# Kernel tuning notes

Measured on AMD Instinct MI355X. Metric: run time of the kernel, lower is better.

## Reference

```python
import jax, jax.numpy as jnp
import numpy as np

N, E = 50000, 800000
IN, HID, OUT, K = 500, 128, 128, 10
BN_EPS = 1e-5


def _encode(x, src, dst, norm, n, W_in, b_in, gam, high_pass, bn_scale, bn_shift, W_up, b_up):
    # input projection (dropout_p = 0 -> identity)
    h = x @ W_in + b_in  # [N, HID]

    def prop(t):
        # symmetric-normalized sparse matvec: (D^-1/2 A D^-1/2) t
        return jax.ops.segment_sum(norm[:, None] * t[src], dst, num_segments=n)

    def step(carry, g):
        t, acc = carry
        acc = acc + g * t
        pt = prop(t)
        # low-pass basis: A_hat^k x ; high-pass basis: (I - A_hat)^k x
        t = (t - pt) if high_pass else pt
        return (t, acc), None

    (_, acc), _ = jax.lax.scan(step, (h, jnp.zeros_like(h)), gam)

    # BatchNorm1d over the node axis (training-mode batch statistics)
    mu = acc.mean(axis=0)
    var = acc.var(axis=0)
    hn = (acc - mu) * jax.lax.rsqrt(var + BN_EPS) * bn_scale + bn_shift
    z = hn @ W_up + b_up
    return jax.nn.relu(z)  # act_fn='relu' (PolyGCL default)


def setup_inputs() -> dict:
    key = jax.random.key(0)
    ks = jax.random.split(key, 4)
    x = jax.random.normal(ks[0], (N, IN), dtype=jnp.float32)
    edge_index = jax.random.randint(ks[1], (2, E), 0, N, dtype=jnp.int32)
    W_in = jax.random.normal(ks[2], (IN, HID), dtype=jnp.float32) * (1.0 / np.sqrt(IN))
    b_in = jnp.zeros((HID,), dtype=jnp.float32)
    # low-pass: decreasing coefficients; high-pass: increasing (PolyGCL init scheme)
    gamma_L = jnp.linspace(2.0, 0.0, K + 1, dtype=jnp.float32)
    gamma_H = jnp.linspace(0.0, 2.0, K + 1, dtype=jnp.float32)
    bn_scale = jnp.ones((HID,), dtype=jnp.float32)
    bn_shift = jnp.zeros((HID,), dtype=jnp.float32)
    W_up = jax.random.normal(ks[3], (HID, OUT), dtype=jnp.float32) * (1.0 / np.sqrt(HID))
    b_up = jnp.zeros((OUT,), dtype=jnp.float32)
    return {"x": x, "edge_index": edge_index, "W_in": W_in, "b_in": b_in,
            "gamma_L": gamma_L, "gamma_H": gamma_H,
            "bn_scale": bn_scale, "bn_shift": bn_shift,
            "W_up": W_up, "b_up": b_up}


def reference(x, edge_index, W_in, b_in, gamma_L, gamma_H, bn_scale, bn_shift, W_up, b_up):
    n = x.shape[0]
    src, dst = edge_index[0], edge_index[1]
    deg = jax.ops.segment_sum(jnp.ones(src.shape, dtype=x.dtype), dst, num_segments=n)
    dinv = jax.lax.rsqrt(jnp.maximum(deg, 1.0))
    norm = dinv[src] * dinv[dst]  # [E]
    Z_L = _encode(x, src, dst, norm, n, W_in, b_in, gamma_L, False, bn_scale, bn_shift, W_up, b_up)
    Z_H = _encode(x, src, dst, norm, n, W_in, b_in, gamma_H, True, bn_scale, bn_shift, W_up, b_up)
    return (Z_L, Z_H)
```

## Files before the change

kernel.cpp:

```cpp
#include <hip/hip_runtime.h>
#include <hip/hip_fp16.h>

#define HIDF 128

typedef float v4f __attribute__((ext_vector_type(4)));
typedef _Float16 half8 __attribute__((ext_vector_type(8)));
typedef float f32x4 __attribute__((ext_vector_type(4)));
struct alignas(8) half4 { __half2 lo, hi; };

static inline int cdiv(int a, int b) { return (a + b - 1) / b; }
static inline size_t alup(size_t b) { return (b + 255) & ~(size_t)255; }

__global__ void k_deg(const int* __restrict__ dst, int E, int* __restrict__ deg) {
    int i = blockIdx.x * blockDim.x + threadIdx.x;
    if (i < E) atomicAdd(&deg[dst[i]], 1);
}

__global__ void k_coef(const float* __restrict__ gL, const float* __restrict__ gH, int K,
                       float* __restrict__ cL, float* __restrict__ cH) {
    if (threadIdx.x == 0 && blockIdx.x == 0) {
        for (int j = 0; j <= K; ++j) {
            double s = 0.0;
            double C = 1.0;
            for (int k = j; k <= K; ++k) {
                s += (double)gH[k] * C;
                C = C * (double)(k + 1) / (double)(k + 1 - j);
            }
            cH[j] = (j & 1) ? (float)(-s) : (float)s;
            cL[j] = gL[j];
        }
    }
}

__global__ __launch_bounds__(256) void k_scan1(const int* __restrict__ deg, int N,
                                               int* __restrict__ bsum,
                                               float* __restrict__ dinv) {
    __shared__ int ls[256];
    int tid = threadIdx.x;
    int i = blockIdx.x * 256 + tid;
    int v = 0;
    if (i < N) {
        v = deg[i];
        dinv[i] = rsqrtf(fmaxf((float)v, 1.0f));
    }
    ls[tid] = v;
    __syncthreads();
    for (int off = 128; off > 0; off >>= 1) {
        if (tid < off) ls[tid] += ls[tid + off];
        __syncthreads();
    }
    if (tid == 0) bsum[blockIdx.x] = ls[0];
}

__global__ __launch_bounds__(1024) void k_scan2(int* __restrict__ bsum, int nb) {
    __shared__ int ls[1024];
    int tid = threadIdx.x;
    int v = (tid < nb) ? bsum[tid] : 0;
    ls[tid] = v;
    __syncthreads();
    for (int off = 1; off < 1024; off <<= 1) {
        int t = (tid >= off) ? ls[tid - off] : 0;
        __syncthreads();
        ls[tid] += t;
        __syncthreads();
    }
    if (tid < nb) bsum[tid] = ls[tid] - v;
}

__global__ __launch_bounds__(256) void k_scan3(const int* __restrict__ deg,
                                               const int* __restrict__ bsum, int N,
                                               int* __restrict__ row_ptr) {
    __shared__ int ls[256];
    int tid = threadIdx.x;
    int i = blockIdx.x * 256 + tid;
    int v = (i < N) ? deg[i] : 0;
    ls[tid] = v;
    __syncthreads();
    for (int off = 1; off < 256; off <<= 1) {
        int t = (tid >= off) ? ls[tid - off] : 0;
        __syncthreads();
        ls[tid] += t;
        __syncthreads();
    }
    if (i <= N) row_ptr[i] = bsum[blockIdx.x] + ls[tid] - v;
}

__global__ __launch_bounds__(1024) void k_scan(const int* __restrict__ deg, int N,
                                               int* __restrict__ row_ptr,
                                               float* __restrict__ dinv) {
    __shared__ int ls[1024];
    int tid = threadIdx.x;
    int chunk = (N + 1023) / 1024;
    int start = tid * chunk;
    int end = min(start + chunk, N);
    int s = 0;
    for (int i = start; i < end; ++i) {
        int d = deg[i];
        s += d;
        dinv[i] = rsqrtf(fmaxf((float)d, 1.0f));
    }
    ls[tid] = s;
    __syncthreads();
    for (int off = 1; off < 1024; off <<= 1) {
        int v = (tid >= off) ? ls[tid - off] : 0;
        __syncthreads();
        ls[tid] += v;
        __syncthreads();
    }
    int run = ls[tid] - s;
    for (int i = start; i < end; ++i) {
        row_ptr[i] = run;
        run += deg[i];
    }
    if (tid == 1023) row_ptr[N] = run;
}

__global__ void k_scatter(const int* __restrict__ src, const int* __restrict__ dst, int E,
                          const int* __restrict__ row_ptr, int* __restrict__ fill,
                          const float* __restrict__ dinv, int* __restrict__ csr_src,
                          float* __restrict__ csr_w) {
    int i = blockIdx.x * blockDim.x + threadIdx.x;
    if (i < E) {
        int s = src[i], d = dst[i];
        int pos = row_ptr[d] + atomicAdd(&fill[d], 1);
        csr_src[pos] = s;
        csr_w[pos] = dinv[s] * dinv[d];
    }
}

__global__ __launch_bounds__(512) void k_wprep(const float* __restrict__ W, int Kdim, int KP,
                                               _Float16* __restrict__ Wh,
                                               _Float16* __restrict__ Wl) {
    int i = blockIdx.x * blockDim.x + threadIdx.x;
    int total = 128 * KP;
    if (i >= total) return;
    int n = i / KP;
    int k = i - n * KP;
    float w = (k < Kdim) ? W[(long)k * HIDF + n] : 0.0f;
    _Float16 h = (_Float16)w;
    _Float16 l = (_Float16)(w - (float)h);
    Wh[(long)n * KP + k] = h;
    Wl[(long)n * KP + k] = l;
}

__global__ __launch_bounds__(512) void k_gemm_in_mfma(
    const float* __restrict__ X, const _Float16* __restrict__ Wh,
    const _Float16* __restrict__ Wl, const float* __restrict__ b, __half* __restrict__ U0,
    int M, int Kdim, int KP) {
    __shared__ _Float16 Ah[128][40];
    __shared__ _Float16 Al[128][40];
    __shared__ _Float16 Bh[128][40];
    __shared__ _Float16 Bl[128][40];
    int tid = threadIdx.x;
    int lane = tid & 63;
    int wid = tid >> 6;
    int wr = wid >> 1;
    int wc = wid & 1;
    int lr = lane & 15;
    int kq = lane >> 4;
    int kof = kq * 8;
    int row0 = blockIdx.x * 128;
    int sm = tid >> 2;
    int kk = (tid & 3) * 8;
    bool k4ok = ((Kdim & 3) == 0);

    f32x4 acc[2][4] = {};

    for (int k0 = 0; k0 < KP; k0 += 32) {
        *(half8*)&Bh[sm][kk] = *(const half8*)&Wh[(long)sm * KP + k0 + kk];
        *(half8*)&Bl[sm][kk] = *(const half8*)&Wl[(long)sm * KP + k0 + kk];
        {
            int r = row0 + sm;
            int gk = k0 + kk;
            half8 hv, lv;
            if (r < M && (gk + 8) <= Kdim && k4ok) {
                float4 v0 = *(const float4*)&X[(long)r * Kdim + gk];
                float4 v1 = *(const float4*)&X[(long)r * Kdim + gk + 4];
                float xs[8] = {v0.x, v0.y, v0.z, v0.w, v1.x, v1.y, v1.z, v1.w};
#pragma unroll
                for (int j = 0; j < 8; ++j) {
                    _Float16 h = (_Float16)xs[j];
                    hv[j] = h;
                    lv[j] = (_Float16)(xs[j] - (float)h);
                }
            } else {
#pragma unroll
                for (int j = 0; j < 8; ++j) {
                    float x = (r < M && (gk + j) < Kdim) ? X[(long)r * Kdim + gk + j] : 0.0f;
                    _Float16 h = (_Float16)x;
                    hv[j] = h;
                    lv[j] = (_Float16)(x - (float)h);
                }
            }
            *(half8*)&Ah[sm][kk] = hv;
            *(half8*)&Al[sm][kk] = lv;
        }
        __syncthreads();

        half8 a_h0 = *(const half8*)&Ah[wr * 32 + lr][kof];
        half8 a_h1 = *(const half8*)&Ah[wr * 32 + 16 + lr][kof];
        half8 a_l0 = *(const half8*)&Al[wr * 32 + lr][kof];
        half8 a_l1 = *(const half8*)&Al[wr * 32 + 16 + lr][kof];
#pragma unroll
        for (int cg = 0; cg < 4; ++cg) {
            half8 b_h = *(const half8*)&Bh[wc * 64 + cg * 16 + lr][kof];
            half8 b_l = *(const half8*)&Bl[wc * 64 + cg * 16 + lr][kof];
            acc[0][cg] = __builtin_amdgcn_mfma_f32_16x16x32_f16(a_h0, b_h, acc[0][cg], 0, 0, 0);
            acc[1][cg] = __builtin_amdgcn_mfma_f32_16x16x32_f16(a_h1, b_h, acc[1][cg], 0, 0, 0);
            acc[0][cg] = __builtin_amdgcn_mfma_f32_16x16x32_f16(a_l0, b_h, acc[0][cg], 0, 0, 0);
            acc[1][cg] = __builtin_amdgcn_mfma_f32_16x16x32_f16(a_l1, b_h, acc[1][cg], 0, 0, 0);
            acc[0][cg] = __builtin_amdgcn_mfma_f32_16x16x32_f16(a_h0, b_l, acc[0][cg], 0, 0, 0);
            acc[1][cg] = __builtin_amdgcn_mfma_f32_16x16x32_f16(a_h1, b_l, acc[1][cg], 0, 0, 0);
        }
        __syncthreads();
    }

    float bb[4];
#pragma unroll
    for (int cg = 0; cg < 4; ++cg) bb[cg] = b[wc * 64 + cg * 16 + lr];
#pragma unroll
    for (int i = 0; i < 2; ++i) {
#pragma unroll
        for (int j = 0; j < 4; ++j) {
            int r = row0 + wr * 32 + i * 16 + kq * 4 + j;
            if (r < M) {
#pragma unroll
                for (int cg = 0; cg < 4; ++cg) {
                    int n = wc * 64 + cg * 16 + lr;
                    U0[(long)r * HIDF + n] = __float2half(acc[i][cg][j] + bb[cg]);
                }
            }
        }
    }
}

__global__ __launch_bounds__(512) void k_gemm_up_mfma(
    const float* __restrict__ accL, const float* __restrict__ accH,
    const _Float16* __restrict__ Wh, const _Float16* __restrict__ Wl,
    const float* __restrict__ bias, const float* __restrict__ a_mul,
    const float* __restrict__ aaW, float* __restrict__ out, int M) {
    int enc = blockIdx.y;
    const float* A = enc ? accH : accL;
    float* O = out + (size_t)enc * M * HIDF;
    __shared__ _Float16 Ah[128][40];
    __shared__ _Float16 Al[128][40];
    __shared__ _Float16 Bh[128][40];
    __shared__ _Float16 Bl[128][40];
    __shared__ float ams[128];
    int tid = threadIdx.x;
    int lane = tid & 63;
    int wid = tid >> 6;
    int wr = wid >> 1;
    int wc = wid & 1;
    int lr = lane & 15;
    int kq = lane >> 4;
    int kof = kq * 8;
    int row0 = blockIdx.x * 128;
    int sm = tid >> 2;
    int kk = (tid & 3) * 8;
    if (tid < 128) ams[tid] = a_mul[enc * 128 + tid];
    __syncthreads();

    f32x4 acc[2][4] = {};

    for (int k0 = 0; k0 < 128; k0 += 32) {
        *(half8*)&Bh[sm][kk] = *(const half8*)&Wh[(long)sm * 128 + k0 + kk];
        *(half8*)&Bl[sm][kk] = *(const half8*)&Wl[(long)sm * 128 + k0 + kk];
        {
            int r = row0 + sm;
            half8 hv, lv;
            if (r < M) {
                float4 v0 = *(const float4*)&A[(long)r * 128 + k0 + kk];
                float4 v1 = *(const float4*)&A[(long)r * 128 + k0 + kk + 4];
                float xs[8] = {v0.x, v0.y, v0.z, v0.w, v1.x, v1.y, v1.z, v1.w};
#pragma unroll
                for (int j = 0; j < 8; ++j) {
                    float sv = xs[j] * ams[k0 + kk + j];
                    _Float16 h = (_Float16)sv;
                    hv[j] = h;
                    lv[j] = (_Float16)(sv - (float)h);
                }
            } else {
#pragma unroll
                for (int j = 0; j < 8; ++j) { hv[j] = (_Float16)0.f; lv[j] = (_Float16)0.f; }
            }
            *(half8*)&Ah[sm][kk] = hv;
            *(half8*)&Al[sm][kk] = lv;
        }
        __syncthreads();

        half8 a_h0 = *(const half8*)&Ah[wr * 32 + lr][kof];
        half8 a_h1 = *(const half8*)&Ah[wr * 32 + 16 + lr][kof];
        half8 a_l0 = *(const half8*)&Al[wr * 32 + lr][kof];
        half8 a_l1 = *(const half8*)&Al[wr * 32 + 16 + lr][kof];
#pragma unroll
        for (int cg = 0; cg < 4; ++cg) {
            half8 b_h = *(const half8*)&Bh[wc * 64 + cg * 16 + lr][kof];
            half8 b_l = *(const half8*)&Bl[wc * 64 + cg * 16 + lr][kof];
            acc[0][cg] = __builtin_amdgcn_mfma_f32_16x16x32_f16(a_h0, b_h, acc[0][cg], 0, 0, 0);
            acc[1][cg] = __builtin_amdgcn_mfma_f32_16x16x32_f16(a_h1, b_h, acc[1][cg], 0, 0, 0);
            acc[0][cg] = __builtin_amdgcn_mfma_f32_16x16x32_f16(a_l0, b_h, acc[0][cg], 0, 0, 0);
            acc[1][cg] = __builtin_amdgcn_mfma_f32_16x16x32_f16(a_l1, b_h, acc[1][cg], 0, 0, 0);
            acc[0][cg] = __builtin_amdgcn_mfma_f32_16x16x32_f16(a_h0, b_l, acc[0][cg], 0, 0, 0);
            acc[1][cg] = __builtin_amdgcn_mfma_f32_16x16x32_f16(a_h1, b_l, acc[1][cg], 0, 0, 0);
        }
        __syncthreads();
    }

    float bb[4];
#pragma unroll
    for (int cg = 0; cg < 4; ++cg) {
        int n = wc * 64 + cg * 16 + lr;
        bb[cg] = bias[n] + aaW[enc * 128 + n];
    }
#pragma unroll
    for (int i = 0; i < 2; ++i) {
#pragma unroll
        for (int j = 0; j < 4; ++j) {
            int r = row0 + wr * 32 + i * 16 + kq * 4 + j;
            if (r < M) {
#pragma unroll
                for (int cg = 0; cg < 4; ++cg) {
                    int n = wc * 64 + cg * 16 + lr;
                    O[(long)r * HIDF + n] = fmaxf(acc[i][cg][j] + bb[cg], 0.0f);
                }
            }
        }
    }
}

__global__ __launch_bounds__(512) void k_gemm_in_f(
    const float* __restrict__ X, const float* __restrict__ W, const float* __restrict__ b,
    float* __restrict__ H, float* __restrict__ accL, float* __restrict__ accH,
    const float* __restrict__ cL, const float* __restrict__ cH, int M, int Kdim) {
    const int BK = 20;
    __shared__ float As[BK][132];
    __shared__ float Bs[BK][128];
    int tid = threadIdx.x;
    int tx = tid & 31, ty = tid >> 5;
    int row0 = blockIdx.x * 128;
    float acc[8][4] = {};
    for (int k0 = 0; k0 < Kdim; k0 += BK) {
        for (int l = tid; l < 640; l += 512) {
            int m = l / 5, q = l % 5;
            int r = row0 + m;
            float4 v = {0.f, 0.f, 0.f, 0.f};
            if (r < M) v = *(const float4*)&X[(long)r * Kdim + k0 + q * 4];
            As[q * 4 + 0][m] = v.x;
            As[q * 4 + 1][m] = v.y;
            As[q * 4 + 2][m] = v.z;
            As[q * 4 + 3][m] = v.w;
        }
        for (int l = tid; l < 640; l += 512) {
            int k = l >> 5, n = (l & 31) * 4;
            *(float4*)&Bs[k][n] = *(const float4*)&W[(long)(k0 + k) * 128 + n];
        }
        __syncthreads();
#pragma unroll
        for (int k = 0; k < BK; ++k) {
            float4 a0 = *(const float4*)&As[k][ty * 8];
            float4 a1 = *(const float4*)&As[k][ty * 8 + 4];
            float4 bb = *(const float4*)&Bs[k][tx * 4];
            float a[8] = {a0.x, a0.y, a0.z, a0.w, a1.x, a1.y, a1.z, a1.w};
#pragma unroll
            for (int i = 0; i < 8; ++i) {
                acc[i][0] += a[i] * bb.x;
                acc[i][1] += a[i] * bb.y;
                acc[i][2] += a[i] * bb.z;
                acc[i][3] += a[i] * bb.w;
            }
        }
        __syncthreads();
    }
    float g0 = cL[0], h0 = cH[0];
    float4 bias = *(const float4*)&b[tx * 4];
    float bv[4] = {bias.x, bias.y, bias.z, bias.w};
#pragma unroll
    for (int i = 0; i < 8; ++i) {
        int r = row0 + ty * 8 + i;
        if (r < M) {
            long idx = (long)r * 128 + tx * 4;
            float4 vh;
            float* ph = (float*)&vh;
#pragma unroll
            for (int j = 0; j < 4; ++j) ph[j] = acc[i][j] + bv[j];
            *(float4*)&H[idx] = vh;
            float4 vl = {g0 * vh.x, g0 * vh.y, g0 * vh.z, g0 * vh.w};
            float4 vv = {h0 * vh.x, h0 * vh.y, h0 * vh.z, h0 * vh.w};
            *(float4*)&accL[idx] = vl;
            *(float4*)&accH[idx] = vv;
        }
    }
}

__global__ __launch_bounds__(256) void k_prop_h(
    const int* __restrict__ row_ptr, const int* __restrict__ csr_src,
    const float* __restrict__ csr_w, const __half* __restrict__ t_in,
    __half* __restrict__ t_out, int N) {
    int wave = threadIdx.x >> 6;
    int lane = threadIdx.x & 63;
    int half = lane >> 5;
    int l5 = lane & 31;
    int node = blockIdx.x * 4 + wave;
    if (node >= N) return;
    int e0 = row_ptr[node], e1 = row_ptr[node + 1];
    float sx = 0.f, sy = 0.f, sz = 0.f, sw = 0.f;
    int e = e0 + half;
    for (; e + 14 < e1; e += 16) {
        int idx[8];
        float w[8];
        half4 v[8];
#pragma unroll
        for (int q = 0; q < 8; ++q) {
            idx[q] = csr_src[e + 2 * q];
            w[q] = csr_w[e + 2 * q];
        }
#pragma unroll
        for (int q = 0; q < 8; ++q) v[q] = *(const half4*)&t_in[(long)idx[q] * HIDF + l5 * 4];
#pragma unroll
        for (int q = 0; q < 8; ++q) {
            float2 a = __half22float2(v[q].lo), b2 = __half22float2(v[q].hi);
            sx += w[q] * a.x;
            sy += w[q] * a.y;
            sz += w[q] * b2.x;
            sw += w[q] * b2.y;
        }
    }
    for (; e + 6 < e1; e += 8) {
        int idx[4];
        float w[4];
        half4 v[4];
#pragma unroll
        for (int q = 0; q < 4; ++q) {
            idx[q] = csr_src[e + 2 * q];
            w[q] = csr_w[e + 2 * q];
        }
#pragma unroll
        for (int q = 0; q < 4; ++q) v[q] = *(const half4*)&t_in[(long)idx[q] * HIDF + l5 * 4];
#pragma unroll
        for (int q = 0; q < 4; ++q) {
            float2 a = __half22float2(v[q].lo), b2 = __half22float2(v[q].hi);
            sx += w[q] * a.x;
            sy += w[q] * a.y;
            sz += w[q] * b2.x;
            sw += w[q] * b2.y;
        }
    }
    for (; e < e1; e += 2) {
        int i0 = csr_src[e];
        float w0 = csr_w[e];
        half4 v0 = *(const half4*)&t_in[(long)i0 * HIDF + l5 * 4];
        float2 a0 = __half22float2(v0.lo), b0 = __half22float2(v0.hi);
        sx += w0 * a0.x;
        sy += w0 * a0.y;
        sz += w0 * b0.x;
        sw += w0 * b0.y;
    }
    sx += __shfl_xor(sx, 32);
    sy += __shfl_xor(sy, 32);
    sz += __shfl_xor(sz, 32);
    sw += __shfl_xor(sw, 32);
    if (half == 0) {
        half4 o;
        o.lo = __float22half2_rn(make_float2(sx, sy));
        o.hi = __float22half2_rn(make_float2(sz, sw));
        *(half4*)&t_out[(long)node * HIDF + l5 * 4] = o;
    }
}

__global__ __launch_bounds__(256) void k_prop(
    const int* __restrict__ row_ptr, const int* __restrict__ csr_src,
    const float* __restrict__ csr_w, const float* __restrict__ t_in,
    float* __restrict__ t_out, float* __restrict__ accL, float* __restrict__ accH,
    const float* __restrict__ cL, const float* __restrict__ cH, int j, int N, int write_t) {
    int wave = threadIdx.x >> 6;
    int lane = threadIdx.x & 63;
    int half = lane >> 5;
    int l5 = lane & 31;
    int node = blockIdx.x * 4 + wave;
    if (node >= N) return;
    int e0 = row_ptr[node], e1 = row_ptr[node + 1];
    float sx = 0.f, sy = 0.f, sz = 0.f, sw = 0.f;
    int e = e0 + half;
    for (; e + 6 < e1; e += 8) {
        int i0 = csr_src[e], i1 = csr_src[e + 2], i2 = csr_src[e + 4], i3 = csr_src[e + 6];
        float w0 = csr_w[e], w1 = csr_w[e + 2], w2 = csr_w[e + 4], w3 = csr_w[e + 6];
        float4 v0 = *(const float4*)&t_in[(long)i0 * HIDF + l5 * 4];
        float4 v1 = *(const float4*)&t_in[(long)i1 * HIDF + l5 * 4];
        float4 v2 = *(const float4*)&t_in[(long)i2 * HIDF + l5 * 4];
        float4 v3 = *(const float4*)&t_in[(long)i3 * HIDF + l5 * 4];
        sx += w0 * v0.x + w1 * v1.x + w2 * v2.x + w3 * v3.x;
        sy += w0 * v0.y + w1 * v1.y + w2 * v2.y + w3 * v3.y;
        sz += w0 * v0.z + w1 * v1.z + w2 * v2.z + w3 * v3.z;
        sw += w0 * v0.w + w1 * v1.w + w2 * v2.w + w3 * v3.w;
    }
    for (; e < e1; e += 2) {
        int i0 = csr_src[e];
        float w0 = csr_w[e];
        float4 v0 = *(const float4*)&t_in[(long)i0 * HIDF + l5 * 4];
        sx += w0 * v0.x;
        sy += w0 * v0.y;
        sz += w0 * v0.z;
        sw += w0 * v0.w;
    }
    sx += __shfl_xor(sx, 32);
    sy += __shfl_xor(sy, 32);
    sz += __shfl_xor(sz, 32);
    sw += __shfl_xor(sw, 32);
    if (half == 0) {
        long base = (long)node * HIDF + l5 * 4;
        if (write_t) {
            float4 o = {sx, sy, sz, sw};
            *(float4*)&t_out[base] = o;
        }
        float gL = cL[j], gH = cH[j];
        float4 aL = *(const float4*)&accL[base];
        float4 aH = *(const float4*)&accH[base];
        aL.x += gL * sx; aL.y += gL * sy; aL.z += gL * sz; aL.w += gL * sw;
        aH.x += gH * sx; aH.y += gH * sy; aH.z += gH * sz; aH.w += gH * sw;
        *(float4*)&accL[base] = aL;
        *(float4*)&accH[base] = aH;
    }
}

__global__ __launch_bounds__(256) void k_combine_h2(
    const __half* __restrict__ tb, long tstride, int K, float* __restrict__ accL,
    float* __restrict__ accH, const float* __restrict__ cL, const float* __restrict__ cH,
    int N, float* __restrict__ sums) {
    int tid = threadIdx.x;
    int fg = tid & 15;
    int rg = tid >> 4;
    int lane = tid & 63;
    int wid = tid >> 6;
    float s1[8] = {}, s2[8] = {}, s3[8] = {}, s4[8] = {};

    if (K == 10) {
        float gl[11], gh[11];
#pragma unroll
        for (int j = 0; j < 11; ++j) {
            gl[j] = cL[j];
            gh[j] = cH[j];
        }
        for (long r = (long)blockIdx.x * 16 + rg; r < N; r += (long)gridDim.x * 16) {
            const __half* p = tb + r * HIDF + fg * 8;
            half8 v[11];
#pragma unroll
            for (int j = 0; j < 11; ++j) v[j] = *(const half8*)(p + (long)j * tstride);
            float aL[8] = {}, aH[8] = {};
#pragma unroll
            for (int j = 0; j < 11; ++j) {
#pragma unroll
                for (int e = 0; e < 8; ++e) {
                    float t = (float)v[j][e];
                    aL[e] += gl[j] * t;
                    aH[e] += gh[j] * t;
                }
            }
            long base = r * HIDF + fg * 8;
            float4 o0 = {aL[0], aL[1], aL[2], aL[3]};
            float4 o1 = {aL[4], aL[5], aL[6], aL[7]};
            float4 o2 = {aH[0], aH[1], aH[2], aH[3]};
            float4 o3 = {aH[4], aH[5], aH[6], aH[7]};
            *(float4*)&accL[base] = o0;
            *(float4*)&accL[base + 4] = o1;
            *(float4*)&accH[base] = o2;
            *(float4*)&accH[base + 4] = o3;
#pragma unroll
            for (int e = 0; e < 8; ++e) {
                s1[e] += aL[e];
                s2[e] += aL[e] * aL[e];
                s3[e] += aH[e];
                s4[e] += aH[e] * aH[e];
            }
        }
    } else {
        for (long r = (long)blockIdx.x * 16 + rg; r < N; r += (long)gridDim.x * 16) {
            const __half* p = tb + r * HIDF + fg * 8;
            float aL[8] = {}, aH[8] = {};
            for (int j = 0; j <= K; ++j) {
                half8 v = *(const half8*)(p + (long)j * tstride);
                float gL = cL[j], gH = cH[j];
#pragma unroll
                for (int e = 0; e < 8; ++e) {
                    float t = (float)v[e];
                    aL[e] += gL * t;
                    aH[e] += gH * t;
                }
            }
            long base = r * HIDF + fg * 8;
            float4 o0 = {aL[0], aL[1], aL[2], aL[3]};
            float4 o1 = {aL[4], aL[5], aL[6], aL[7]};
            float4 o2 = {aH[0], aH[1], aH[2], aH[3]};
            float4 o3 = {aH[4], aH[5], aH[6], aH[7]};
            *(float4*)&accL[base] = o0;
            *(float4*)&accL[base + 4] = o1;
            *(float4*)&accH[base] = o2;
            *(float4*)&accH[base + 4] = o3;
#pragma unroll
            for (int e = 0; e < 8; ++e) {
                s1[e] += aL[e];
                s2[e] += aL[e] * aL[e];
                s3[e] += aH[e];
                s4[e] += aH[e] * aH[e];
            }
        }
    }

#pragma unroll
    for (int e = 0; e < 8; ++e) {
        s1[e] += __shfl_xor(s1[e], 16); s1[e] += __shfl_xor(s1[e], 32);
        s2[e] += __shfl_xor(s2[e], 16); s2[e] += __shfl_xor(s2[e], 32);
        s3[e] += __shfl_xor(s3[e], 16); s3[e] += __shfl_xor(s3[e], 32);
        s4[e] += __shfl_xor(s4[e], 16); s4[e] += __shfl_xor(s4[e], 32);
    }
    __shared__ float ls[4][16][32];
    if (lane < 16) {
#pragma unroll
        for (int e = 0; e < 8; ++e) {
            ls[wid][lane][e] = s1[e];
            ls[wid][lane][8 + e] = s2[e];
            ls[wid][lane][16 + e] = s3[e];
            ls[wid][lane][24 + e] = s4[e];
        }
    }
    __syncthreads();
    for (int idx = tid; idx < 512; idx += 256) {
        int f16i = idx >> 5, j = idx & 31;
        float v = ls[0][f16i][j] + ls[1][f16i][j] + ls[2][f16i][j] + ls[3][f16i][j];
        int stat = j >> 3, e = j & 7;
        atomicAdd(&sums[stat * 128 + f16i * 8 + e], v);
    }
}

__global__ __launch_bounds__(256) void k_stats(const float* __restrict__ accL,
                                               const float* __restrict__ accH, int N,
                                               float* __restrict__ sums) {
    int tid = threadIdx.x;
    int l5 = tid & 31;
    int g = tid >> 5;
    float4 l1 = {0, 0, 0, 0}, l2 = {0, 0, 0, 0}, h1 = {0, 0, 0, 0}, h2 = {0, 0, 0, 0};
    for (int r = blockIdx.x * 8 + g; r < N; r += gridDim.x * 8) {
        float4 v = *(const float4*)&accL[(long)r * HIDF + l5 * 4];
        l1.x += v.x; l1.y += v.y; l1.z += v.z; l1.w += v.w;
        l2.x += v.x * v.x; l2.y += v.y * v.y; l2.z += v.z * v.z; l2.w += v.w * v.w;
        float4 u = *(const float4*)&accH[(long)r * HIDF + l5 * 4];
        h1.x += u.x; h1.y += u.y; h1.z += u.z; h1.w += u.w;
        h2.x += u.x * u.x; h2.y += u.y * u.y; h2.z += u.z * u.z; h2.w += u.w * u.w;
    }
    __shared__ float4 s1[256], s2[256], s3[256], s4[256];
    s1[tid] = l1; s2[tid] = l2; s3[tid] = h1; s4[tid] = h2;
    __syncthreads();
    if (tid < 32) {
        float4 a = s1[tid], bq = s2[tid], c = s3[tid], d = s4[tid];
        for (int gg = 1; gg < 8; ++gg) {
            float4 t;
            t = s1[gg * 32 + tid]; a.x += t.x; a.y += t.y; a.z += t.z; a.w += t.w;
            t = s2[gg * 32 + tid]; bq.x += t.x; bq.y += t.y; bq.z += t.z; bq.w += t.w;
            t = s3[gg * 32 + tid]; c.x += t.x; c.y += t.y; c.z += t.z; c.w += t.w;
            t = s4[gg * 32 + tid]; d.x += t.x; d.y += t.y; d.z += t.z; d.w += t.w;
        }
        int f = tid * 4;
        atomicAdd(&sums[f + 0], a.x); atomicAdd(&sums[f + 1], a.y);
        atomicAdd(&sums[f + 2], a.z); atomicAdd(&sums[f + 3], a.w);
        atomicAdd(&sums[128 + f + 0], bq.x); atomicAdd(&sums[128 + f + 1], bq.y);
        atomicAdd(&sums[128 + f + 2], bq.z); atomicAdd(&sums[128 + f + 3], bq.w);
        atomicAdd(&sums[256 + f + 0], c.x); atomicAdd(&sums[256 + f + 1], c.y);
        atomicAdd(&sums[256 + f + 2], c.z); atomicAdd(&sums[256 + f + 3], c.w);
        atomicAdd(&sums[384 + f + 0], d.x); atomicAdd(&sums[384 + f + 1], d.y);
        atomicAdd(&sums[384 + f + 2], d.z); atomicAdd(&sums[384 + f + 3], d.w);
    }
}

__global__ void k_bnfin(const float* __restrict__ sums, int N, const float* __restrict__ scale,
                        const float* __restrict__ shift, const float* __restrict__ Wup,
                        float* __restrict__ a_mul, float* __restrict__ a_add,
                        float* __restrict__ aaW) {
    __shared__ float sh_add[2][128];
    int f = threadIdx.x;
    for (int enc = 0; enc < 2; ++enc) {
        float mu = sums[enc * 256 + f] / (float)N;
        float var = sums[enc * 256 + 128 + f] / (float)N - mu * mu;
        float rstd = rsqrtf(var + 1e-5f);
        float am = rstd * scale[f];
        a_mul[enc * 128 + f] = am;
        float ad = shift[f] - mu * am;
        a_add[enc * 128 + f] = ad;
        sh_add[enc][f] = ad;
    }
    __syncthreads();
    int n = f;
    float s0 = 0.f, s1 = 0.f;
    for (int ff = 0; ff < 128; ++ff) {
        float w = Wup[ff * 128 + n];
        s0 += sh_add[0][ff] * w;
        s1 += sh_add[1][ff] * w;
    }
    aaW[n] = s0;
    aaW[128 + n] = s1;
}

extern "C" void kernel_launch(void* const* d_in, const int* in_sizes, int n_in, void* d_out,
                              int out_size, void* d_ws, size_t ws_size, hipStream_t stream) {
    const float* x = (const float*)d_in[0];
    const int* edge_index = (const int*)d_in[1];
    const float* W_in = (const float*)d_in[2];
    const float* b_in = (const float*)d_in[3];
    const float* gamma_L = (const float*)d_in[4];
    const float* gamma_H = (const float*)d_in[5];
    const float* bn_scale = (const float*)d_in[6];
    const float* bn_shift = (const float*)d_in[7];
    const float* W_up = (const float*)d_in[8];
    const float* b_up = (const float*)d_in[9];
    float* out = (float*)d_out;

    const int HID = in_sizes[3];
    const int IN = in_sizes[2] / HID;
    const int N = in_sizes[0] / IN;
    const int E = in_sizes[1] / 2;
    const int K = in_sizes[4] - 1;

    const int* src = edge_index;
    const int* dst = edge_index + E;

    const int KP = (IN + 31) & ~31;

    char* base = (char*)d_ws;
    size_t off = 0;
    auto take = [&](size_t bytes) -> char* {
        char* r = base + off;
        off += alup(bytes);
        return r;
    };
    int* deg = (int*)take((size_t)N * 4);
    int* row_ptr = (int*)take((size_t)(N + 1) * 4);
    int* fill = (int*)take((size_t)N * 4);
    float* dinv = (float*)take((size_t)N * 4);
    int* bsum = (int*)take(1024 * 4);
    int* csr_src = (int*)take((size_t)E * 4);
    float* csr_w = (float*)take((size_t)E * 4);
    float* accL = (float*)take((size_t)N * HID * 4);
    float* accH = (float*)take((size_t)N * HID * 4);
    float* sums = (float*)take(512 * 4);
    float* cL = (float*)take(64 * 4);
    float* cH = (float*)take(64 * 4);
    float* a_mul = (float*)take(256 * 4);
    float* a_add = (float*)take(256 * 4);
    float* aaW = (float*)take(256 * 4);
    _Float16* Wt_h = (_Float16*)take((size_t)HID * KP * 2);
    _Float16* Wt_l = (_Float16*)take((size_t)HID * KP * 2);
    _Float16* Wup_h = (_Float16*)take((size_t)HID * HID * 2);
    _Float16* Wup_l = (_Float16*)take((size_t)HID * HID * 2);

    size_t per16 = alup((size_t)N * HID * 2);
    long stride16 = (long)(per16 / 2);
    __half* tb16 = (__half*)(base + off);
    bool deferred = (off + (size_t)(K + 1) * per16) <= ws_size && K < 60;
    size_t per32 = alup((size_t)N * HID * 4);
    long stride32 = (long)(per32 / 4);
    float* fb = (float*)(base + off);
    if (!deferred && off + 2 * per32 > ws_size) deferred = true;

    hipMemsetAsync(deg, 0, (size_t)N * 4, stream);
    hipMemsetAsync(fill, 0, (size_t)N * 4, stream);
    hipMemsetAsync(sums, 0, 512 * 4, stream);

    k_coef<<<1, 64, 0, stream>>>(gamma_L, gamma_H, K, cL, cH);
    k_deg<<<cdiv(E, 256), 256, 0, stream>>>(dst, E, deg);

    int nb = cdiv(N + 1, 256);
    if (nb <= 1024) {
        k_scan1<<<nb, 256, 0, stream>>>(deg, N, bsum, dinv);
        k_scan2<<<1, 1024, 0, stream>>>(bsum, nb);
        k_scan3<<<nb, 256, 0, stream>>>(deg, bsum, N, row_ptr);
    } else {
        k_scan<<<1, 1024, 0, stream>>>(deg, N, row_ptr, dinv);
    }

    k_scatter<<<cdiv(E, 256), 256, 0, stream>>>(src, dst, E, row_ptr, fill, dinv, csr_src,
                                                csr_w);
    k_wprep<<<cdiv(HID * HID, 512), 512, 0, stream>>>(W_up, HID, HID, Wup_h, Wup_l);

    if (deferred) {
        k_wprep<<<cdiv(HID * KP, 512), 512, 0, stream>>>(W_in, IN, KP, Wt_h, Wt_l);
        k_gemm_in_mfma<<<cdiv(N, 128), 512, 0, stream>>>(x, Wt_h, Wt_l, b_in, tb16, N, IN, KP);
        for (int j = 1; j <= K; ++j) {
            const __half* tin = tb16 + (long)(j - 1) * stride16;
            __half* tout = tb16 + (long)j * stride16;
            k_prop_h<<<cdiv(N, 4), 256, 0, stream>>>(row_ptr, csr_src, csr_w, tin, tout, N);
        }
        k_combine_h2<<<512, 256, 0, stream>>>(tb16, stride16, K, accL, accH, cL, cH, N, sums);
    } else {
        float* h = fb;
        float* ta = fb + stride32;
        k_gemm_in_f<<<cdiv(N, 128), 512, 0, stream>>>(x, W_in, b_in, h, accL, accH, cL, cH,
                                                      N, IN);
        const float* tin = h;
        float* tout = ta;
        for (int j = 1; j <= K; ++j) {
            int write_t = (j < K) ? 1 : 0;
            k_prop<<<cdiv(N, 4), 256, 0, stream>>>(row_ptr, csr_src, csr_w, tin, tout, accL,
                                                   accH, cL, cH, j, N, write_t);
            const float* nt = tout;
            tout = (nt == ta) ? h : ta;
            tin = nt;
        }
        k_stats<<<200, 256, 0, stream>>>(accL, accH, N, sums);
    }

    k_bnfin<<<1, 128, 0, stream>>>(sums, N, bn_scale, bn_shift, W_up, a_mul, a_add, aaW);
    dim3 gup(cdiv(N, 128), 2);
    k_gemm_up_mfma<<<gup, 512, 0, stream>>>(accL, accH, Wup_h, Wup_l, b_up, a_mul, aaW, out,
                                            N);
}
```

Measured before the change: 682.7 us.

## Double-buffer LDS tiles in input and output MFMA GEMMs with register prefetch

Both split-fp16 MFMA GEMM kernels now keep two LDS buffers. The next K-tile is prefetched from global memory into registers while MFMAs run on the current tile, and the loop needs one barrier per iteration instead of two. This is meant to hide global load latency behind compute. In exchange, LDS use per block doubles to about 80KB, which may lower occupancy, and live register count rises.

```diff
diff --git a/kernel.cpp b/kernel.cpp
--- a/kernel.cpp
+++ b/kernel.cpp
@@ -147,10 +147,10 @@
     const float* __restrict__ X, const _Float16* __restrict__ Wh,
     const _Float16* __restrict__ Wl, const float* __restrict__ b, __half* __restrict__ U0,
     int M, int Kdim, int KP) {
-    __shared__ _Float16 Ah[128][40];
-    __shared__ _Float16 Al[128][40];
-    __shared__ _Float16 Bh[128][40];
-    __shared__ _Float16 Bl[128][40];
+    __shared__ _Float16 Ah[2][128][40];
+    __shared__ _Float16 Al[2][128][40];
+    __shared__ _Float16 Bh[2][128][40];
+    __shared__ _Float16 Bl[2][128][40];
     int tid = threadIdx.x;
     int lane = tid & 63;
     int wid = tid >> 6;
@@ -163,48 +163,49 @@
     int sm = tid >> 2;
     int kk = (tid & 3) * 8;
     bool k4ok = ((Kdim & 3) == 0);
+    int r_st = row0 + sm;
 
     f32x4 acc[2][4] = {};
-
-    for (int k0 = 0; k0 < KP; k0 += 32) {
-        *(half8*)&Bh[sm][kk] = *(const half8*)&Wh[(long)sm * KP + k0 + kk];
-        *(half8*)&Bl[sm][kk] = *(const half8*)&Wl[(long)sm * KP + k0 + kk];
-        {
-            int r = row0 + sm;
-            int gk = k0 + kk;
-            half8 hv, lv;
-            if (r < M && (gk + 8) <= Kdim && k4ok) {
-                float4 v0 = *(const float4*)&X[(long)r * Kdim + gk];
-                float4 v1 = *(const float4*)&X[(long)r * Kdim + gk + 4];
-                float xs[8] = {v0.x, v0.y, v0.z, v0.w, v1.x, v1.y, v1.z, v1.w};
-#pragma unroll
-                for (int j = 0; j < 8; ++j) {
-                    _Float16 h = (_Float16)xs[j];
-                    hv[j] = h;
-                    lv[j] = (_Float16)(xs[j] - (float)h);
-                }
-            } else {
-#pragma unroll
-                for (int j = 0; j < 8; ++j) {
-                    float x = (r < M && (gk + j) < Kdim) ? X[(long)r * Kdim + gk + j] : 0.0f;
-                    _Float16 h = (_Float16)x;
-                    hv[j] = h;
-                    lv[j] = (_Float16)(x - (float)h);
-                }
-            }
-            *(half8*)&Ah[sm][kk] = hv;
-            *(half8*)&Al[sm][kk] = lv;
-        }
-        __syncthreads();
-
-        half8 a_h0 = *(const half8*)&Ah[wr * 32 + lr][kof];
-        half8 a_h1 = *(const half8*)&Ah[wr * 32 + 16 + lr][kof];
-        half8 a_l0 = *(const half8*)&Al[wr * 32 + lr][kof];
-        half8 a_l1 = *(const half8*)&Al[wr * 32 + 16 + lr][kof];
+    float xs[8];
+    half8 wbh, wbl;
+
+    auto LOAD = [&](int k0) {
+        wbh = *(const half8*)&Wh[(long)sm * KP + k0 + kk];
+        wbl = *(const half8*)&Wl[(long)sm * KP + k0 + kk];
+        int gk = k0 + kk;
+        if (r_st < M && k4ok && (gk + 8) <= Kdim) {
+            float4 v0 = *(const float4*)&X[(long)r_st * Kdim + gk];
+            float4 v1 = *(const float4*)&X[(long)r_st * Kdim + gk + 4];
+            xs[0] = v0.x; xs[1] = v0.y; xs[2] = v0.z; xs[3] = v0.w;
+            xs[4] = v1.x; xs[5] = v1.y; xs[6] = v1.z; xs[7] = v1.w;
+        } else {
+#pragma unroll
+            for (int j = 0; j < 8; ++j)
+                xs[j] = (r_st < M && (gk + j) < Kdim) ? X[(long)r_st * Kdim + gk + j] : 0.0f;
+        }
+    };
+    auto WRITE = [&](int buf) {
+        half8 hv, lv;
+#pragma unroll
+        for (int j = 0; j < 8; ++j) {
+            _Float16 h = (_Float16)xs[j];
+            hv[j] = h;
+            lv[j] = (_Float16)(xs[j] - (float)h);
+        }
+        *(half8*)&Ah[buf][sm][kk] = hv;
+        *(half8*)&Al[buf][sm][kk] = lv;
+        *(half8*)&Bh[buf][sm][kk] = wbh;
+        *(half8*)&Bl[buf][sm][kk] = wbl;
+    };
+    auto COMPUTE = [&](int buf) {
+        half8 a_h0 = *(const half8*)&Ah[buf][wr * 32 + lr][kof];
+        half8 a_h1 = *(const half8*)&Ah[buf][wr * 32 + 16 + lr][kof];
+        half8 a_l0 = *(const half8*)&Al[buf][wr * 32 + lr][kof];
+        half8 a_l1 = *(const half8*)&Al[buf][wr * 32 + 16 + lr][kof];
 #pragma unroll
         for (int cg = 0; cg < 4; ++cg) {
-            half8 b_h = *(const half8*)&Bh[wc * 64 + cg * 16 + lr][kof];
-            half8 b_l = *(const half8*)&Bl[wc * 64 + cg * 16 + lr][kof];
+            half8 b_h = *(const half8*)&Bh[buf][wc * 64 + cg * 16 + lr][kof];
+            half8 b_l = *(const half8*)&Bl[buf][wc * 64 + cg * 16 + lr][kof];
             acc[0][cg] = __builtin_amdgcn_mfma_f32_16x16x32_f16(a_h0, b_h, acc[0][cg], 0, 0, 0);
             acc[1][cg] = __builtin_amdgcn_mfma_f32_16x16x32_f16(a_h1, b_h, acc[1][cg], 0, 0, 0);
             acc[0][cg] = __builtin_amdgcn_mfma_f32_16x16x32_f16(a_l0, b_h, acc[0][cg], 0, 0, 0);
@@ -212,7 +213,21 @@
             acc[0][cg] = __builtin_amdgcn_mfma_f32_16x16x32_f16(a_h0, b_l, acc[0][cg], 0, 0, 0);
             acc[1][cg] = __builtin_amdgcn_mfma_f32_16x16x32_f16(a_h1, b_l, acc[1][cg], 0, 0, 0);
         }
-        __syncthreads();
+    };
+
+    const int NT = KP / 32;
+    LOAD(0);
+    WRITE(0);
+    __syncthreads();
+    int cur = 0;
+    for (int t = 0; t < NT; ++t) {
+        if (t + 1 < NT) LOAD((t + 1) * 32);
+        COMPUTE(cur);
+        if (t + 1 < NT) {
+            WRITE(cur ^ 1);
+            __syncthreads();
+            cur ^= 1;
+        }
     }
 
     float bb[4];
@@ -242,10 +257,10 @@
     int enc = blockIdx.y;
     const float* A = enc ? accH : accL;
     float* O = out + (size_t)enc * M * HIDF;
-    __shared__ _Float16 Ah[128][40];
-    __shared__ _Float16 Al[128][40];
-    __shared__ _Float16 Bh[128][40];
-    __shared__ _Float16 Bl[128][40];
+    __shared__ _Float16 Ah[2][128][40];
+    __shared__ _Float16 Al[2][128][40];
+    __shared__ _Float16 Bh[2][128][40];
+    __shared__ _Float16 Bl[2][128][40];
     __shared__ float ams[128];
     int tid = threadIdx.x;
     int lane = tid & 63;
@@ -258,45 +273,52 @@
     int row0 = blockIdx.x * 128;
     int sm = tid >> 2;
     int kk = (tid & 3) * 8;
+    int r_st = row0 + sm;
     if (tid < 128) ams[tid] = a_mul[enc * 128 + tid];
     __syncthreads();
 
     f32x4 acc[2][4] = {};
-
-    for (int k0 = 0; k0 < 128; k0 += 32) {
-        *(half8*)&Bh[sm][kk] = *(const half8*)&Wh[(long)sm * 128 + k0 + kk];
-        *(half8*)&Bl[sm][kk] = *(const half8*)&Wl[(long)sm * 128 + k0 + kk];
-        {
-            int r = row0 + sm;
-            half8 hv, lv;
-            if (r < M) {
-                float4 v0 = *(const float4*)&A[(long)r * 128 + k0 + kk];
-                float4 v1 = *(const float4*)&A[(long)r * 128 + k0 + kk + 4];
-                float xs[8] = {v0.x, v0.y, v0.z, v0.w, v1.x, v1.y, v1.z, v1.w};
-#pragma unroll
-                for (int j = 0; j < 8; ++j) {
-                    float sv = xs[j] * ams[k0 + kk + j];
-                    _Float16 h = (_Float16)sv;
-                    hv[j] = h;
-                    lv[j] = (_Float16)(sv - (float)h);
-                }
-            } else {
-#pragma unroll
-                for (int j = 0; j < 8; ++j) { hv[j] = (_Float16)0.f; lv[j] = (_Float16)0.f; }
-            }
-            *(half8*)&Ah[sm][kk] = hv;
-            *(half8*)&Al[sm][kk] = lv;
-        }
-        __syncthreads();
-
-        half8 a_h0 = *(const half8*)&Ah[wr * 32 + lr][kof];
-        half8 a_h1 = *(const half8*)&Ah[wr * 32 + 16 + lr][kof];
-        half8 a_l0 = *(const half8*)&Al[wr * 32 + lr][kof];
-        half8 a_l1 = *(const half8*)&Al[wr * 32 + 16 + lr][kof];
+    float xs[8];
+    half8 wbh, wbl;
+    int pk0 = 0;
+
+    auto LOAD = [&](int k0) {
+        pk0 = k0;
+        wbh = *(const half8*)&Wh[(long)sm * 128 + k0 + kk];
+        wbl = *(const half8*)&Wl[(long)sm * 128 + k0 + kk];
+        if (r_st < M) {
+            float4 v0 = *(const float4*)&A[(long)r_st * 128 + k0 + kk];
+            float4 v1 = *(const float4*)&A[(long)r_st * 128 + k0 + kk + 4];
+            xs[0] = v0.x; xs[1] = v0.y; xs[2] = v0.z; xs[3] = v0.w;
+            xs[4] = v1.x; xs[5] = v1.y; xs[6] = v1.z; xs[7] = v1.w;
+        } else {
+#pragma unroll
+            for (int j = 0; j < 8; ++j) xs[j] = 0.0f;
+        }
+    };
+    auto WRITE = [&](int buf) {
+        half8 hv, lv;
+#pragma unroll
+        for (int j = 0; j < 8; ++j) {
+            float sv = xs[j] * ams[pk0 + kk + j];
+            _Float16 h = (_Float16)sv;
+            hv[j] = h;
+            lv[j] = (_Float16)(sv - (float)h);
+        }
+        *(half8*)&Ah[buf][sm][kk] = hv;
+        *(half8*)&Al[buf][sm][kk] = lv;
+        *(half8*)&Bh[buf][sm][kk] = wbh;
+        *(half8*)&Bl[buf][sm][kk] = wbl;
+    };
+    auto COMPUTE = [&](int buf) {
+        half8 a_h0 = *(const half8*)&Ah[buf][wr * 32 + lr][kof];
+        half8 a_h1 = *(const half8*)&Ah[buf][wr * 32 + 16 + lr][kof];
+        half8 a_l0 = *(const half8*)&Al[buf][wr * 32 + lr][kof];
+        half8 a_l1 = *(const half8*)&Al[buf][wr * 32 + 16 + lr][kof];
 #pragma unroll
         for (int cg = 0; cg < 4; ++cg) {
-            half8 b_h = *(const half8*)&Bh[wc * 64 + cg * 16 + lr][kof];
-            half8 b_l = *(const half8*)&Bl[wc * 64 + cg * 16 + lr][kof];
+            half8 b_h = *(const half8*)&Bh[buf][wc * 64 + cg * 16 + lr][kof];
+            half8 b_l = *(const half8*)&Bl[buf][wc * 64 + cg * 16 + lr][kof];
             acc[0][cg] = __builtin_amdgcn_mfma_f32_16x16x32_f16(a_h0, b_h, acc[0][cg], 0, 0, 0);
             acc[1][cg] = __builtin_amdgcn_mfma_f32_16x16x32_f16(a_h1, b_h, acc[1][cg], 0, 0, 0);
             acc[0][cg] = __builtin_amdgcn_mfma_f32_16x16x32_f16(a_l0, b_h, acc[0][cg], 0, 0, 0);
@@ -304,7 +326,21 @@
             acc[0][cg] = __builtin_amdgcn_mfma_f32_16x16x32_f16(a_h0, b_l, acc[0][cg], 0, 0, 0);
             acc[1][cg] = __builtin_amdgcn_mfma_f32_16x16x32_f16(a_h1, b_l, acc[1][cg], 0, 0, 0);
         }
-        __syncthreads();
+    };
+
+    const int NT = 4;
+    LOAD(0);
+    WRITE(0);
+    __syncthreads();
+    int cur = 0;
+    for (int t = 0; t < NT; ++t) {
+        if (t + 1 < NT) LOAD((t + 1) * 32);
+        COMPUTE(cur);
+        if (t + 1 < NT) {
+            WRITE(cur ^ 1);
+            __syncthreads();
+            cur ^= 1;
+        }
     }
 
     float bb[4];
```

New measurement: 694.5 us. About the same (+1.7%).

## Map 16 lanes per node in fp16 propagation with 16-byte gathers and index prefetch

Applied to the files above, without the earlier changes.

The fp16 SpMM propagation kernel now gives each node 16 lanes (four nodes per wavefront), with each lane loading eight halves per neighbor instead of four. This removes the half-wave split and the cross-half shuffle reduction. The next batch of eight neighbor indices and weights is loaded while the current batch is being gathered. Lanes of the same wave now walk different degree counts, so uneven degrees within a wave can cause divergence, and register pressure rises.

```diff
diff --git a/kernel.cpp b/kernel.cpp
--- a/kernel.cpp
+++ b/kernel.cpp
@@ -397,75 +397,68 @@
     const int* __restrict__ row_ptr, const int* __restrict__ csr_src,
     const float* __restrict__ csr_w, const __half* __restrict__ t_in,
     __half* __restrict__ t_out, int N) {
-    int wave = threadIdx.x >> 6;
-    int lane = threadIdx.x & 63;
-    int half = lane >> 5;
-    int l5 = lane & 31;
-    int node = blockIdx.x * 4 + wave;
+    int tid = threadIdx.x;
+    int lane = tid & 63;
+    int wid = tid >> 6;
+    int slot = lane >> 4;
+    int l4 = lane & 15;
+    int node = blockIdx.x * 16 + wid * 4 + slot;
     if (node >= N) return;
     int e0 = row_ptr[node], e1 = row_ptr[node + 1];
-    float sx = 0.f, sy = 0.f, sz = 0.f, sw = 0.f;
-    int e = e0 + half;
-    for (; e + 14 < e1; e += 16) {
-        int idx[8];
-        float w[8];
-        half4 v[8];
+    float acc[8] = {};
+    int e = e0;
+    int nb = (e1 - e0) >> 3;
+
+    int idxA[8];
+    float wA[8];
+    if (nb > 0) {
 #pragma unroll
         for (int q = 0; q < 8; ++q) {
-            idx[q] = csr_src[e + 2 * q];
-            w[q] = csr_w[e + 2 * q];
-        }
-#pragma unroll
-        for (int q = 0; q < 8; ++q) v[q] = *(const half4*)&t_in[(long)idx[q] * HIDF + l5 * 4];
+            idxA[q] = csr_src[e + q];
+            wA[q] = csr_w[e + q];
+        }
+    }
+    for (int bb = 0; bb < nb; ++bb) {
+        half8 v[8];
+#pragma unroll
+        for (int q = 0; q < 8; ++q)
+            v[q] = *(const half8*)&t_in[(long)idxA[q] * HIDF + l4 * 8];
+        int en = e + 8;
+        bool more = (bb + 1 < nb);
+        int idxB[8];
+        float wB[8];
+        if (more) {
+#pragma unroll
+            for (int q = 0; q < 8; ++q) {
+                idxB[q] = csr_src[en + q];
+                wB[q] = csr_w[en + q];
+            }
+        }
 #pragma unroll
         for (int q = 0; q < 8; ++q) {
-            float2 a = __half22float2(v[q].lo), b2 = __half22float2(v[q].hi);
-            sx += w[q] * a.x;
-            sy += w[q] * a.y;
-            sz += w[q] * b2.x;
-            sw += w[q] * b2.y;
-        }
-    }
-    for (; e + 6 < e1; e += 8) {
-        int idx[4];
-        float w[4];
-        half4 v[4];
-#pragma unroll
-        for (int q = 0; q < 4; ++q) {
-            idx[q] = csr_src[e + 2 * q];
-            w[q] = csr_w[e + 2 * q];
-        }
-#pragma unroll
-        for (int q = 0; q < 4; ++q) v[q] = *(const half4*)&t_in[(long)idx[q] * HIDF + l5 * 4];
-#pragma unroll
-        for (int q = 0; q < 4; ++q) {
-            float2 a = __half22float2(v[q].lo), b2 = __half22float2(v[q].hi);
-            sx += w[q] * a.x;
-            sy += w[q] * a.y;
-            sz += w[q] * b2.x;
-            sw += w[q] * b2.y;
-        }
-    }
-    for (; e < e1; e += 2) {
+#pragma unroll
+            for (int f = 0; f < 8; ++f) acc[f] += wA[q] * (float)v[q][f];
+        }
+        if (more) {
+#pragma unroll
+            for (int q = 0; q < 8; ++q) {
+                idxA[q] = idxB[q];
+                wA[q] = wB[q];
+            }
+        }
+        e = en;
+    }
+    for (; e < e1; ++e) {
         int i0 = csr_src[e];
         float w0 = csr_w[e];
-        half4 v0 = *(const half4*)&t_in[(long)i0 * HIDF + l5 * 4];
-        float2 a0 = __half22float2(v0.lo), b0 = __half22float2(v0.hi);
-        sx += w0 * a0.x;
-        sy += w0 * a0.y;
-        sz += w0 * b0.x;
-        sw += w0 * b0.y;
-    }
-    sx += __shfl_xor(sx, 32);
-    sy += __shfl_xor(sy, 32);
-    sz += __shfl_xor(sz, 32);
-    sw += __shfl_xor(sw, 32);
-    if (half == 0) {
-        half4 o;
-        o.lo = __float22half2_rn(make_float2(sx, sy));
-        o.hi = __float22half2_rn(make_float2(sz, sw));
-        *(half4*)&t_out[(long)node * HIDF + l5 * 4] = o;
-    }
+        half8 v = *(const half8*)&t_in[(long)i0 * HIDF + l4 * 8];
+#pragma unroll
+        for (int f = 0; f < 8; ++f) acc[f] += w0 * (float)v[f];
+    }
+    half8 o;
+#pragma unroll
+    for (int f = 0; f < 8; ++f) o[f] = (_Float16)acc[f];
+    *(half8*)&t_out[(long)node * HIDF + l4 * 8] = o;
 }
 
 __global__ __launch_bounds__(256) void k_prop(
@@ -786,7 +779,7 @@
         for (int j = 1; j <= K; ++j) {
             const __half* tin = tb16 + (long)(j - 1) * stride16;
             __half* tout = tb16 + (long)j * stride16;
-            k_prop_h<<<cdiv(N, 4), 256, 0, stream>>>(row_ptr, csr_src, csr_w, tin, tout, N);
+            k_prop_h<<<cdiv(N, 16), 256, 0, stream>>>(row_ptr, csr_src, csr_w, tin, tout, N);
         }
         k_combine_h2<<<512, 256, 0, stream>>>(tb16, stride16, K, accL, accH, cL, cH, N, sums);
     } else {
```

After: 720.2 us. 5.5% more time.
